# Performance work log

Measured on AMD Instinct MI355X. Metric: run time of the kernel, lower is better.

## Reference

```python
import jax, jax.numpy as jnp
import numpy as np

B, T, C = 2, 2048, 1024
H, D, R = 16, 64, 32  # heads, head_dim, compression rank (R < D)


def setup_inputs() -> dict:
    key = jax.random.key(0)
    ks = jax.random.split(key, 8)
    s = 0.02
    return {
        "hidden_states": jax.random.normal(ks[0], (B, T, C), jnp.float32),
        "c_attn_w": jax.random.normal(ks[1], (C, 3 * C), jnp.float32) * s,
        "c_attn_b": jnp.zeros((3 * C,), jnp.float32),
        "c_proj_w": jax.random.normal(ks[2], (C, C), jnp.float32) * s,
        "c_proj_b": jnp.zeros((C,), jnp.float32),
        "wk_c": jax.random.normal(ks[3], (D, R), jnp.float32) * (1.0 / np.sqrt(D)),
        "wk_e": jax.random.normal(ks[4], (R, D), jnp.float32) * (1.0 / np.sqrt(R)),
        "wv_c": jax.random.normal(ks[5], (D, R), jnp.float32) * (1.0 / np.sqrt(D)),
        "wv_e": jax.random.normal(ks[6], (R, D), jnp.float32) * (1.0 / np.sqrt(R)),
    }


def reference(hidden_states, c_attn_w, c_attn_b, c_proj_w, c_proj_b,
              wk_c, wk_e, wv_c, wv_e):
    b, t, c = hidden_states.shape
    # GPT2 Conv1D: x @ W + b, then split into Q, K, V
    qkv = hidden_states @ c_attn_w + c_attn_b  # [B,T,3C]
    q, k, v = jnp.split(qkv, 3, axis=-1)

    def split_heads(x):  # [B,T,C] -> [B,H,T,D]
        return x.reshape(b, t, H, D).transpose(0, 2, 1, 3)

    q = split_heads(q)
    k = split_heads(k)
    v = split_heads(v)

    # Low-rank KV compression then expansion (rank R < D path)
    k_lat = jnp.einsum('bhtd,dr->bhtr', k, wk_c)  # [B,H,T,R]
    v_lat = jnp.einsum('bhtd,dr->bhtr', v, wv_c)
    k_exp = jnp.einsum('bhtr,rd->bhtd', k_lat, wk_e)  # [B,H,T,D]
    v_exp = jnp.einsum('bhtr,rd->bhtd', v_lat, wv_e)

    # Causal SDPA (attention_mask is None and q_len > 1 -> is_causal=True)
    scale = 1.0 / np.sqrt(D).astype(np.float32)
    scores = jnp.einsum('bhqd,bhkd->bhqk', q, k_exp) * scale  # [B,H,T,T]
    causal = jnp.tril(jnp.ones((t, t), dtype=bool))
    scores = jnp.where(causal[None, None], scores, jnp.finfo(scores.dtype).min)
    probs = jax.nn.softmax(scores, axis=-1)
    attn = jnp.einsum('bhqk,bhkd->bhqd', probs, v_exp)  # [B,H,T,D]

    # Merge heads and output projection
    attn = attn.transpose(0, 2, 1, 3).reshape(b, t, c)
    out = attn @ c_proj_w + c_proj_b
    return out
```

## Files before the change

### kernel.cpp

```cpp
#include <hip/hip_runtime.h>
#include <cstddef>

typedef __attribute__((ext_vector_type(8))) __bf16 bf16x8;
typedef __attribute__((ext_vector_type(4))) float f32x4;
typedef unsigned short u16;
typedef unsigned int   u32;

#define SCLF (0.125f * 1.44269504f)

__device__ __forceinline__ u16 f2bf(float f){
  union { float f; u32 u; } v; v.f = f;
  u32 r = v.u + 0x7FFFu + ((v.u >> 16) & 1u);
  return (u16)(r >> 16);
}
__device__ __forceinline__ u32 cvtpk(float lo, float hi){
  u32 r; asm("v_cvt_pk_bf16_f32 %0, %1, %2" : "=v"(r) : "v"(lo), "v"(hi)); return r;
}
__device__ __forceinline__ void gll16(const void* g, void* l){
  __builtin_amdgcn_global_load_lds((__attribute__((address_space(1))) void*)g,
                                   (__attribute__((address_space(3))) void*)l, 16, 0, 0);
}

__global__ __launch_bounds__(256) void prep_all(const float* __restrict__ x,
      const float* __restrict__ Wa, const float* __restrict__ ba, const float* __restrict__ Wp,
      const float* __restrict__ kc, const float* __restrict__ ke,
      const float* __restrict__ vc, const float* __restrict__ ve,
      u16* __restrict__ Wt, float* __restrict__ b2, u16* __restrict__ W2t,
      u16* __restrict__ Xb){
  __shared__ __align__(16) char PS[40960];
  const int bid = blockIdx.x, tid = threadIdx.x;
  if (bid < 768){
    float* WaL = (float*)PS;
    float* Ws  = (float*)(PS + 16640);
    const int part = bid >> 8, rem = bid & 255, h = rem >> 4, cc = rem & 15;
    #pragma unroll
    for (int i=0;i<8;++i){
      int idx = tid + i*256; int d = idx>>5, r = idx&31;
      Ws[idx] = (part==0) ? ke[r*64+d] : (part==1) ? kc[idx] : vc[idx];
    }
    const int c0 = cc*64, off = part*1024 + h*64;
    {
      int col = tid & 63, rbase = tid >> 6;
      #pragma unroll
      for (int i=0;i<16;++i){
        int row = i*4 + rbase;
        WaL[row*65 + col] = Wa[(size_t)(c0+row)*3072 + off + col];
      }
    }
    __syncthreads();
    const int c = tid & 63, rg = tid >> 6;
    float acc[8] = {};
    for (int d=0; d<64; ++d){
      float a = WaL[c*65 + d];
      #pragma unroll
      for (int rr=0;rr<8;++rr) acc[rr] += a * Ws[d*32 + rg*8 + rr];
    }
    const float scl = (part==0) ? SCLF : 1.f;
    const int nbase = part*512 + h*32 + rg*8;
    #pragma unroll
    for (int rr=0;rr<8;++rr)
      Wt[(size_t)(nbase+rr)*1024 + c0 + c] = f2bf(acc[rr]*scl);
  } else if (bid < 896){
    float* WpL = (float*)PS;
    float* WeL = (float*)(PS + 32768);
    const int idx2 = bid - 768, jc = idx2 & 7, h = idx2 >> 3;
    #pragma unroll
    for (int i=0;i<32;++i){
      int idx = tid + i*256; int d = idx>>7, jj = idx&127;
      WpL[idx] = Wp[(size_t)(h*64+d)*1024 + jc*128 + jj];
    }
    #pragma unroll
    for (int i=0;i<8;++i) WeL[tid + i*256] = ve[tid + i*256];
    __syncthreads();
    const int jj = tid & 127, rg = tid >> 7;
    float out[16] = {};
    #pragma unroll
    for (int d=0; d<64; ++d){
      float pv = WpL[d*128 + jj];
      #pragma unroll
      for (int rr=0; rr<16; ++rr) out[rr] += WeL[(rg*16+rr)*64 + d] * pv;
    }
    #pragma unroll
    for (int rr=0; rr<16; ++rr)
      W2t[(size_t)(jc*128 + jj)*512 + h*32 + rg*16 + rr] = f2bf(out[rr]);
  } else if (bid < 1920){
    const int i0 = (bid - 896)*1024 + tid;
    #pragma unroll
    for (int t=0;t<4;++t){
      int i = i0 + t*256;
      float4 v = ((const float4*)x)[i];
      ushort4 r; r.x = f2bf(v.x); r.y = f2bf(v.y); r.z = f2bf(v.z); r.w = f2bf(v.w);
      ((ushort4*)Xb)[i] = r;
    }
  } else {
    int n = (bid - 1920)*256 + tid;
    int part = n>>9, h = (n>>5)&15, r = n&31;
    const float* bs = ba + part*1024 + h*64;
    float acc = 0.f;
    for (int d=0;d<64;++d){
      float w = (part==0) ? ke[r*64+d] : (part==1) ? kc[d*32+r] : vc[d*32+r];
      acc += bs[d]*w;
    }
    b2[n] = acc * ((part==0) ? SCLF : 1.f);
  }
}

__global__ __launch_bounds__(256) void v_transpose_lat(const u16* __restrict__ QKV,
      u16* __restrict__ Vt){
  __shared__ u16 tile[64][40];
  int tt = blockIdx.x, bh = blockIdx.y;
  int b = bh>>4, h = bh&15;
  int tid = threadIdx.x;
  int row = tid>>2, cc2 = (tid&3)*8;
  const u16* src = QKV + (size_t)(b*2048 + tt*64 + row)*1536 + 1024 + h*32 + cc2;
  *(uint4*)&tile[row][cc2] = *(const uint4*)src;
  __syncthreads();
  int r = tid>>3, pc = (tid&7)*8;
  u16 vals[8];
  #pragma unroll
  for (int i=0;i<8;++i){
    int p = pc+i; int c = p>>5, q = p&31, g = q>>3, j = q&7;
    int o = c*32 + 16*(j>>2) + 4*g + (j&3);
    vals[i] = tile[o][r];
  }
  u16* drow = Vt + (size_t)(bh*32 + r)*2048 + tt*64 + pc;
  *(uint4*)drow = *(const uint4*)&vals[0];
}

template<typename OT>
__global__ __launch_bounds__(256) void gemm64(const u16* __restrict__ A, const u16* __restrict__ Bt,
        const float* __restrict__ bias, OT* __restrict__ C, int M, int N, int K, int ldc){
  __shared__ u16 As[64*64];
  __shared__ u16 Bs[128*64];
  const int nwg = gridDim.x * gridDim.y;
  const int id  = blockIdx.x + gridDim.x * blockIdx.y;
  const int nid = (id & 7) * (nwg >> 3) + (id >> 3);
  const int bx = nid % gridDim.x, by = nid / gridDim.x;
  const int tid = threadIdx.x, wv = tid>>6, ln = tid&63;
  const int lr = ln&15, g8 = (ln>>4)*8;
  const int m0 = bx*64, n0 = by*128;
  const int wr = (wv>>1)*32, wc = (wv&1)*64;
  const int lrow = ln>>3, lcol = (ln&7)*8;
  f32x4 acc[2][4] = {};
  const int nk = K >> 6;
  for (int kt=0; kt<nk; ++kt){
    #pragma unroll
    for (int it=0; it<6; ++it){
      int chunk = wv*6 + it;
      if (chunk < 8){
        int row = chunk*8 + lrow;
        gll16(A + (size_t)(m0+row)*K + kt*64 + lcol, &As[chunk*512]);
      } else {
        int bc = chunk - 8;
        int row = bc*8 + lrow;
        gll16(Bt + (size_t)(n0+row)*K + kt*64 + lcol, &Bs[bc*512]);
      }
    }
    __syncthreads();
    #pragma unroll
    for (int ks=0; ks<2; ++ks){
      bf16x8 af[2], bfr[4];
      #pragma unroll
      for (int mt=0;mt<2;++mt) af[mt]  = *(const bf16x8*)&As[(wr+mt*16+lr)*64 + ks*32 + g8];
      #pragma unroll
      for (int nt=0;nt<4;++nt) bfr[nt] = *(const bf16x8*)&Bs[(wc+nt*16+lr)*64 + ks*32 + g8];
      #pragma unroll
      for (int mt=0;mt<2;++mt)
        #pragma unroll
        for (int nt=0;nt<4;++nt)
          acc[mt][nt] = __builtin_amdgcn_mfma_f32_16x16x32_bf16(af[mt], bfr[nt], acc[mt][nt], 0,0,0);
    }
    __syncthreads();
  }
  #pragma unroll
  for (int mt=0;mt<2;++mt){
    int row = m0 + wr + mt*16 + 4*(ln>>4);
    #pragma unroll
    for (int nt=0;nt<4;++nt){
      int col = n0 + wc + nt*16 + lr;
      float bv = bias[col];
      #pragma unroll
      for (int r=0;r<4;++r){
        float v = acc[mt][nt][r] + bv;
        if constexpr (sizeof(OT) == 2) C[(size_t)(row+r)*ldc + col] = f2bf(v);
        else                           C[(size_t)(row+r)*ldc + col] = v;
      }
    }
  }
}

__global__ __launch_bounds__(512, 8) void attn_fwd(const u16* __restrict__ QKV,
            const u16* __restrict__ Vt, u16* __restrict__ Out){
  const int bh = blockIdx.x;
  const int qt = 31 - blockIdx.y;
  const int b = bh >> 4, h = bh & 15;
  const int tid = threadIdx.x, wv = tid>>6, ln = tid&63;
  const int sg = wv>>2, wvL = wv&3;
  const int lr = ln&15, gq = ln>>4;
  __shared__ __align__(16) char SMEM[32768];
  u16* KB0 = (u16*)SMEM           + (sg*2    )*2048;
  u16* KB1 = (u16*)SMEM           + (sg*2 + 1)*2048;
  u16* VB0 = (u16*)(SMEM + 16384) + (sg*2    )*2048;
  u16* VB1 = (u16*)(SMEM + 16384) + (sg*2 + 1)*2048;
  const int q0 = qt*64;
  const size_t base = (size_t)(b*2048) * 1536;
  bf16x8 qf = *(const bf16x8*)(QKV + base + (size_t)(q0 + wvL*16 + lr)*1536 + h*32 + gq*8);
  const int qglob = q0 + wvL*16 + lr;
  f32x4 o0 = {}, o1 = {};
  float l_r = 0.f;
  const u16* ksrc = QKV + base + 512 + h*32;
  const u16* vsrc = Vt + (size_t)(bh*32)*2048;

  const int ci = wvL*64 + ln;
  const int rK = ci>>2, cK = 8*((ci&3) ^ (rK&3));
  const int rV = ci>>3, cV = 8*((ci&7) ^ (rV&7));

  int offK[4], offV[2][2];
  #pragma unroll
  for (int nt=0;nt<4;++nt)
    offK[nt] = (nt*16+lr)*64 + ((gq*16) ^ ((lr&3)<<4));
  #pragma unroll
  for (int dt=0;dt<2;++dt)
    #pragma unroll
    for (int c=0;c<2;++c)
      offV[dt][c] = (dt*16+lr)*128 + ((c*64 + gq*16) ^ ((lr&7)<<4));

  if (sg <= qt){
    gll16(ksrc + (size_t)(sg*64 + rK)*1536 + cK, KB0 + wvL*512);
    gll16(vsrc + (size_t)rV*2048 + sg*64 + cV,   VB0 + wvL*512);
  }
  __syncthreads();
  const u16* kp = ksrc + (size_t)(sg*64 + 128 + rK)*1536 + cK;
  const u16* vp = vsrc + (size_t)rV*2048 + sg*64 + 128 + cV;
  const size_t KSTEP = (size_t)128*1536;

  #define ABODY(II, KBC, VBC, KBN, VBN) do { \
    const int kt = 2*(II) + sg; \
    if (kt + 2 <= qt){ \
      gll16(kp, (KBN) + wvL*512); \
      gll16(vp, (VBN) + wvL*512); \
      kp += KSTEP; vp += 128; \
    } \
    if (kt <= qt){ \
      f32x4 s4[4] = {}; \
      __builtin_amdgcn_s_setprio(1); \
      _Pragma("unroll") for (int nt=0;nt<4;++nt){ \
        bf16x8 k0 = *(const bf16x8*)((const char*)(KBC) + offK[nt]); \
        s4[nt] = __builtin_amdgcn_mfma_f32_16x16x32_bf16(k0, qf, s4[nt], 0,0,0); \
      } \
      __builtin_amdgcn_s_setprio(0); \
      if (kt == qt){ \
        const int kv0 = kt*64; \
        _Pragma("unroll") for (int nt=0;nt<4;++nt) \
        _Pragma("unroll") for (int r=0;r<4;++r){ \
          int k = kv0 + nt*16 + 4*gq + r; \
          if (k > qglob) s4[nt][r] = -1e30f; \
        } \
      } \
      float p0,p1,p2,p3,p4,p5,p6,p7; \
      p0=__builtin_amdgcn_exp2f(s4[0][0]); p1=__builtin_amdgcn_exp2f(s4[0][1]); \
      p2=__builtin_amdgcn_exp2f(s4[0][2]); p3=__builtin_amdgcn_exp2f(s4[0][3]); \
      p4=__builtin_amdgcn_exp2f(s4[1][0]); p5=__builtin_amdgcn_exp2f(s4[1][1]); \
      p6=__builtin_amdgcn_exp2f(s4[1][2]); p7=__builtin_amdgcn_exp2f(s4[1][3]); \
      l_r += ((p0+p1)+(p2+p3)) + ((p4+p5)+(p6+p7)); \
      union { u32 u[4]; bf16x8 v; } pa0, pa1; \
      pa0.u[0]=cvtpk(p0,p1); pa0.u[1]=cvtpk(p2,p3); pa0.u[2]=cvtpk(p4,p5); pa0.u[3]=cvtpk(p6,p7); \
      p0=__builtin_amdgcn_exp2f(s4[2][0]); p1=__builtin_amdgcn_exp2f(s4[2][1]); \
      p2=__builtin_amdgcn_exp2f(s4[2][2]); p3=__builtin_amdgcn_exp2f(s4[2][3]); \
      p4=__builtin_amdgcn_exp2f(s4[3][0]); p5=__builtin_amdgcn_exp2f(s4[3][1]); \
      p6=__builtin_amdgcn_exp2f(s4[3][2]); p7=__builtin_amdgcn_exp2f(s4[3][3]); \
      l_r += ((p0+p1)+(p2+p3)) + ((p4+p5)+(p6+p7)); \
      pa1.u[0]=cvtpk(p0,p1); pa1.u[1]=cvtpk(p2,p3); pa1.u[2]=cvtpk(p4,p5); pa1.u[3]=cvtpk(p6,p7); \
      __builtin_amdgcn_s_setprio(1); \
      o0 = __builtin_amdgcn_mfma_f32_16x16x32_bf16(pa0.v, *(const bf16x8*)((const char*)(VBC) + offV[0][0]), o0, 0,0,0); \
      o1 = __builtin_amdgcn_mfma_f32_16x16x32_bf16(pa0.v, *(const bf16x8*)((const char*)(VBC) + offV[1][0]), o1, 0,0,0); \
      o0 = __builtin_amdgcn_mfma_f32_16x16x32_bf16(pa1.v, *(const bf16x8*)((const char*)(VBC) + offV[0][1]), o0, 0,0,0); \
      o1 = __builtin_amdgcn_mfma_f32_16x16x32_bf16(pa1.v, *(const bf16x8*)((const char*)(VBC) + offV[1][1]), o1, 0,0,0); \
      __builtin_amdgcn_s_setprio(0); \
    } \
    __syncthreads(); \
  } while(0)

  const int nmax = (qt + 2) >> 1;
  const int jmax = (nmax + 1) >> 1;
  for (int j = 0; j < jmax; ++j){
    ABODY(2*j,   KB0, VB0, KB1, VB1);
    ABODY(2*j+1, KB1, VB1, KB0, VB0);
  }
  l_r += __shfl_xor(l_r, 16);
  l_r += __shfl_xor(l_r, 32);

  float* MO = (float*)SMEM;
  float* ML = (float*)(SMEM + 12288);
  if (sg == 1){
    #pragma unroll
    for (int r=0;r<4;++r){
      MO[(wvL*16 + 4*gq + r)*34 + lr]      = o0[r];
      MO[(wvL*16 + 4*gq + r)*34 + 16 + lr] = o1[r];
    }
    if (gq == 0) ML[wvL*16 + lr] = l_r;
  }
  __syncthreads();
  if (sg == 0){
    float lS = l_r + ML[wvL*16 + lr];
    float lS_o[4];
    #pragma unroll
    for (int r=0;r<4;++r) lS_o[r] = __shfl(lS, 4*gq + r);
    #pragma unroll
    for (int r=0;r<4;++r){
      int orow = wvL*16 + 4*gq + r;
      float v0 = (o0[r] + MO[orow*34 + lr])      / lS_o[r];
      float v1 = (o1[r] + MO[orow*34 + 16 + lr]) / lS_o[r];
      size_t ob = (size_t)(b*2048 + q0 + orow)*512 + h*32;
      Out[ob + lr]      = f2bf(v0);
      Out[ob + 16 + lr] = f2bf(v1);
    }
  }
}

#define WS_B2   0u
#define WS_WT   8192u
#define WS_W2T  (WS_WT + 3145728u)
#define WS_XB   (WS_W2T + 1048576u)
#define WS_QKV  (WS_XB + 8388608u)
#define WS_VT   (WS_QKV + 12582912u)
#define WS_ATT  (WS_VT + 4194304u)

extern "C" void kernel_launch(void* const* d_in, const int* in_sizes, int n_in,
                              void* d_out, int out_size, void* d_ws, size_t ws_size,
                              hipStream_t stream) {
  const float* x  = (const float*)d_in[0];
  const float* Wa = (const float*)d_in[1];
  const float* ba = (const float*)d_in[2];
  const float* Wp = (const float*)d_in[3];
  const float* bp = (const float*)d_in[4];
  const float* kc = (const float*)d_in[5];
  const float* ke = (const float*)d_in[6];
  const float* vc = (const float*)d_in[7];
  const float* ve = (const float*)d_in[8];
  float* out = (float*)d_out;
  char* ws = (char*)d_ws;
  float* b2  = (float*)(ws + WS_B2);
  u16* Wt    = (u16*)(ws + WS_WT);
  u16* W2t   = (u16*)(ws + WS_W2T);
  u16* Xb    = (u16*)(ws + WS_XB);
  u16* QKVb  = (u16*)(ws + WS_QKV);
  u16* Vt    = (u16*)(ws + WS_VT);
  u16* Att   = (u16*)(ws + WS_ATT);

  prep_all<<<1926, 256, 0, stream>>>(x, Wa, ba, Wp, kc, ke, vc, ve, Wt, b2, W2t, Xb);
  gemm64<u16><<<dim3(64,12), 256, 0, stream>>>(Xb, Wt, b2, QKVb, 4096, 1536, 1024, 1536);
  v_transpose_lat<<<dim3(32,32), 256, 0, stream>>>(QKVb, Vt);
  attn_fwd<<<dim3(32,32), 512, 0, stream>>>(QKVb, Vt, Att);
  gemm64<float><<<dim3(64,8), 256, 0, stream>>>(Att, W2t, bp, out, 4096, 1024, 512, 1024);
}
```

Baseline: 86.20 us.

## Fuse fp32-to-bf16 input conversion into QKV GEMM and split prep kernel

Drops the separate conversion of the fp32 hidden states to a bf16 workspace buffer. The QKV GEMM now loads fp32 rows directly, packs them to bf16 in registers and stores them into LDS, while B tiles still use direct global-to-LDS loads. The monolithic prep kernel is split into three kernels for the weight folds and bias fold, with vectorized float4 loads and an LDS-staged bias fold. This saves an 8 MB write and reread of the converted input. In exchange the GEMM reads twice as many A bytes per tile through registers instead of async LDS loads, and there are two extra kernel launches.

```diff
diff --git a/kernel.cpp b/kernel.cpp
--- a/kernel.cpp
+++ b/kernel.cpp
@@ -21,87 +21,112 @@
                                    (__attribute__((address_space(3))) void*)l, 16, 0, 0);
 }
 
-__global__ __launch_bounds__(256) void prep_all(const float* __restrict__ x,
-      const float* __restrict__ Wa, const float* __restrict__ ba, const float* __restrict__ Wp,
+__global__ __launch_bounds__(256) void fold_qkv(const float* __restrict__ Wa,
       const float* __restrict__ kc, const float* __restrict__ ke,
-      const float* __restrict__ vc, const float* __restrict__ ve,
-      u16* __restrict__ Wt, float* __restrict__ b2, u16* __restrict__ W2t,
-      u16* __restrict__ Xb){
-  __shared__ __align__(16) char PS[40960];
-  const int bid = blockIdx.x, tid = threadIdx.x;
-  if (bid < 768){
-    float* WaL = (float*)PS;
-    float* Ws  = (float*)(PS + 16640);
-    const int part = bid >> 8, rem = bid & 255, h = rem >> 4, cc = rem & 15;
-    #pragma unroll
-    for (int i=0;i<8;++i){
-      int idx = tid + i*256; int d = idx>>5, r = idx&31;
-      Ws[idx] = (part==0) ? ke[r*64+d] : (part==1) ? kc[idx] : vc[idx];
-    }
-    const int c0 = cc*64, off = part*1024 + h*64;
-    {
-      int col = tid & 63, rbase = tid >> 6;
-      #pragma unroll
-      for (int i=0;i<16;++i){
-        int row = i*4 + rbase;
-        WaL[row*65 + col] = Wa[(size_t)(c0+row)*3072 + off + col];
-      }
-    }
-    __syncthreads();
-    const int c = tid & 63, rg = tid >> 6;
-    float acc[8] = {};
+      const float* __restrict__ vc, u16* __restrict__ Wt){
+  __shared__ float WaL[64*65];
+  __shared__ float Ws[2048];
+  const int bid = blockIdx.x;
+  const int part = bid >> 8, rem = bid & 255, h = rem >> 4, cc = rem & 15;
+  const int tid = threadIdx.x;
+  {
+    const float* msrc = (part==0) ? ke : (part==1) ? kc : vc;
+    *(float4*)&Ws[tid*4]        = ((const float4*)msrc)[tid];
+    *(float4*)&Ws[1024 + tid*4] = ((const float4*)msrc)[tid + 256];
+  }
+  const int c0 = cc*64, off = part*1024 + h*64;
+  {
+    int r0 = tid >> 4, c4 = (tid & 15) * 4;
+    #pragma unroll
+    for (int i=0;i<4;++i){
+      int row = i*16 + r0;
+      float4 v = *(const float4*)&Wa[(size_t)(c0+row)*3072 + off + c4];
+      WaL[row*65 + c4 + 0] = v.x;
+      WaL[row*65 + c4 + 1] = v.y;
+      WaL[row*65 + c4 + 2] = v.z;
+      WaL[row*65 + c4 + 3] = v.w;
+    }
+  }
+  __syncthreads();
+  const int c = tid & 63, rg = tid >> 6;
+  float acc[8] = {};
+  if (part == 0){
     for (int d=0; d<64; ++d){
       float a = WaL[c*65 + d];
       #pragma unroll
+      for (int rr=0;rr<8;++rr) acc[rr] += a * Ws[(rg*8+rr)*64 + d];
+    }
+  } else {
+    for (int d=0; d<64; ++d){
+      float a = WaL[c*65 + d];
+      #pragma unroll
       for (int rr=0;rr<8;++rr) acc[rr] += a * Ws[d*32 + rg*8 + rr];
     }
-    const float scl = (part==0) ? SCLF : 1.f;
-    const int nbase = part*512 + h*32 + rg*8;
-    #pragma unroll
-    for (int rr=0;rr<8;++rr)
-      Wt[(size_t)(nbase+rr)*1024 + c0 + c] = f2bf(acc[rr]*scl);
-  } else if (bid < 896){
-    float* WpL = (float*)PS;
-    float* WeL = (float*)(PS + 32768);
-    const int idx2 = bid - 768, jc = idx2 & 7, h = idx2 >> 3;
-    #pragma unroll
-    for (int i=0;i<32;++i){
-      int idx = tid + i*256; int d = idx>>7, jj = idx&127;
-      WpL[idx] = Wp[(size_t)(h*64+d)*1024 + jc*128 + jj];
-    }
-    #pragma unroll
-    for (int i=0;i<8;++i) WeL[tid + i*256] = ve[tid + i*256];
-    __syncthreads();
-    const int jj = tid & 127, rg = tid >> 7;
-    float out[16] = {};
-    #pragma unroll
-    for (int d=0; d<64; ++d){
-      float pv = WpL[d*128 + jj];
-      #pragma unroll
-      for (int rr=0; rr<16; ++rr) out[rr] += WeL[(rg*16+rr)*64 + d] * pv;
-    }
-    #pragma unroll
-    for (int rr=0; rr<16; ++rr)
-      W2t[(size_t)(jc*128 + jj)*512 + h*32 + rg*16 + rr] = f2bf(out[rr]);
-  } else if (bid < 1920){
-    const int i0 = (bid - 896)*1024 + tid;
-    #pragma unroll
-    for (int t=0;t<4;++t){
-      int i = i0 + t*256;
-      float4 v = ((const float4*)x)[i];
-      ushort4 r; r.x = f2bf(v.x); r.y = f2bf(v.y); r.z = f2bf(v.z); r.w = f2bf(v.w);
-      ((ushort4*)Xb)[i] = r;
-    }
-  } else {
-    int n = (bid - 1920)*256 + tid;
-    int part = n>>9, h = (n>>5)&15, r = n&31;
-    const float* bs = ba + part*1024 + h*64;
+  }
+  const float scl = (part==0) ? SCLF : 1.f;
+  const int nbase = part*512 + h*32 + rg*8;
+  #pragma unroll
+  for (int rr=0;rr<8;++rr)
+    Wt[(size_t)(nbase+rr)*1024 + c0 + c] = f2bf(acc[rr]*scl);
+}
+
+__global__ __launch_bounds__(256) void fold_proj(const float* __restrict__ Wp,
+      const float* __restrict__ ve, u16* __restrict__ W2t){
+  __shared__ float WpL[8192];
+  __shared__ float WeL[2048];
+  const int jc = blockIdx.x, h = blockIdx.y;
+  const int tid = threadIdx.x;
+  {
+    int dd = tid >> 5, c4 = (tid & 31) * 4;
+    #pragma unroll
+    for (int i=0;i<8;++i){
+      int d = i*8 + dd;
+      *(float4*)&WpL[d*128 + c4] = *(const float4*)&Wp[(size_t)(h*64+d)*1024 + jc*128 + c4];
+    }
+    *(float4*)&WeL[tid*4]        = ((const float4*)ve)[tid];
+    *(float4*)&WeL[1024 + tid*4] = ((const float4*)ve)[tid + 256];
+  }
+  __syncthreads();
+  const int jj = tid & 127, rg = tid >> 7;
+  float out[16] = {};
+  for (int d=0; d<64; ++d){
+    float pv = WpL[d*128 + jj];
+    #pragma unroll
+    for (int rr=0; rr<16; ++rr) out[rr] += WeL[(rg*16+rr)*64 + d] * pv;
+  }
+  #pragma unroll
+  for (int rr=0; rr<16; ++rr)
+    W2t[(size_t)(jc*128 + jj)*512 + h*32 + rg*16 + rr] = f2bf(out[rr]);
+}
+
+__global__ __launch_bounds__(256) void fold_bias(const float* __restrict__ ba,
+      const float* __restrict__ kc, const float* __restrict__ ke,
+      const float* __restrict__ vc, float* __restrict__ b2){
+  __shared__ float BaL[1024];
+  __shared__ float Ws65[32*65];
+  const int part = blockIdx.x, tid = threadIdx.x;
+  *(float4*)&BaL[tid*4] = *(const float4*)&ba[part*1024 + tid*4];
+  {
+    const float* msrc = (part==0) ? ke : (part==1) ? kc : vc;
+    #pragma unroll
+    for (int i=0;i<8;++i){
+      int idx = tid + i*256;
+      float v = msrc[idx];
+      int r, d;
+      if (part == 0){ r = idx >> 6; d = idx & 63; }
+      else          { d = idx >> 5; r = idx & 31; }
+      Ws65[r*65 + d] = v;
+    }
+  }
+  __syncthreads();
+  const float scl = (part==0) ? SCLF : 1.f;
+  #pragma unroll
+  for (int t=0;t<2;++t){
+    int l = tid + t*256;
+    int hh = l >> 5, r = l & 31;
     float acc = 0.f;
-    for (int d=0;d<64;++d){
-      float w = (part==0) ? ke[r*64+d] : (part==1) ? kc[d*32+r] : vc[d*32+r];
-      acc += bs[d]*w;
-    }
-    b2[n] = acc * ((part==0) ? SCLF : 1.f);
+    for (int d=0;d<64;++d) acc += BaL[hh*64 + d] * Ws65[r*65 + d];
+    b2[part*512 + l] = acc * scl;
   }
 }
 
@@ -127,8 +152,8 @@
   *(uint4*)drow = *(const uint4*)&vals[0];
 }
 
-template<typename OT>
-__global__ __launch_bounds__(256) void gemm64(const u16* __restrict__ A, const u16* __restrict__ Bt,
+template<typename AT, typename OT>
+__global__ __launch_bounds__(256) void gemm64(const AT* __restrict__ A, const u16* __restrict__ Bt,
         const float* __restrict__ bias, OT* __restrict__ C, int M, int N, int K, int ldc){
   __shared__ u16 As[64*64];
   __shared__ u16 Bs[128*64];
@@ -144,16 +169,36 @@
   f32x4 acc[2][4] = {};
   const int nk = K >> 6;
   for (int kt=0; kt<nk; ++kt){
-    #pragma unroll
-    for (int it=0; it<6; ++it){
-      int chunk = wv*6 + it;
-      if (chunk < 8){
-        int row = chunk*8 + lrow;
-        gll16(A + (size_t)(m0+row)*K + kt*64 + lcol, &As[chunk*512]);
-      } else {
-        int bc = chunk - 8;
-        int row = bc*8 + lrow;
-        gll16(Bt + (size_t)(n0+row)*K + kt*64 + lcol, &Bs[bc*512]);
+    if constexpr (sizeof(AT) == 4){
+      int row = tid>>2, seg = (tid&3)*16;
+      const float* xs = (const float*)A + (size_t)(m0+row)*K + kt*64 + seg;
+      float4 a0 = ((const float4*)xs)[0], a1 = ((const float4*)xs)[1],
+             a2 = ((const float4*)xs)[2], a3 = ((const float4*)xs)[3];
+      uint4 w0, w1;
+      w0.x = cvtpk(a0.x,a0.y); w0.y = cvtpk(a0.z,a0.w);
+      w0.z = cvtpk(a1.x,a1.y); w0.w = cvtpk(a1.z,a1.w);
+      w1.x = cvtpk(a2.x,a2.y); w1.y = cvtpk(a2.z,a2.w);
+      w1.z = cvtpk(a3.x,a3.y); w1.w = cvtpk(a3.z,a3.w);
+      *(uint4*)&As[row*64 + seg]     = w0;
+      *(uint4*)&As[row*64 + seg + 8] = w1;
+      #pragma unroll
+      for (int it=0; it<4; ++it){
+        int bc = wv*4 + it;
+        int rowb = bc*8 + lrow;
+        gll16(Bt + (size_t)(n0+rowb)*K + kt*64 + lcol, &Bs[bc*512]);
+      }
+    } else {
+      #pragma unroll
+      for (int it=0; it<6; ++it){
+        int chunk = wv*6 + it;
+        if (chunk < 8){
+          int row = chunk*8 + lrow;
+          gll16((const u16*)A + (size_t)(m0+row)*K + kt*64 + lcol, &As[chunk*512]);
+        } else {
+          int bc = chunk - 8;
+          int row = bc*8 + lrow;
+          gll16(Bt + (size_t)(n0+row)*K + kt*64 + lcol, &Bs[bc*512]);
+        }
       }
     }
     __syncthreads();
@@ -321,8 +366,7 @@
 #define WS_B2   0u
 #define WS_WT   8192u
 #define WS_W2T  (WS_WT + 3145728u)
-#define WS_XB   (WS_W2T + 1048576u)
-#define WS_QKV  (WS_XB + 8388608u)
+#define WS_QKV  (WS_W2T + 1048576u)
 #define WS_VT   (WS_QKV + 12582912u)
 #define WS_ATT  (WS_VT + 4194304u)
 
@@ -343,14 +387,15 @@
   float* b2  = (float*)(ws + WS_B2);
   u16* Wt    = (u16*)(ws + WS_WT);
   u16* W2t   = (u16*)(ws + WS_W2T);
-  u16* Xb    = (u16*)(ws + WS_XB);
   u16* QKVb  = (u16*)(ws + WS_QKV);
   u16* Vt    = (u16*)(ws + WS_VT);
   u16* Att   = (u16*)(ws + WS_ATT);
 
-  prep_all<<<1926, 256, 0, stream>>>(x, Wa, ba, Wp, kc, ke, vc, ve, Wt, b2, W2t, Xb);
-  gemm64<u16><<<dim3(64,12), 256, 0, stream>>>(Xb, Wt, b2, QKVb, 4096, 1536, 1024, 1536);
+  fold_bias<<<3, 256, 0, stream>>>(ba, kc, ke, vc, b2);
+  fold_proj<<<dim3(8,16), 256, 0, stream>>>(Wp, ve, W2t);
+  fold_qkv<<<768, 256, 0, stream>>>(Wa, kc, ke, vc, Wt);
+  gemm64<float,u16><<<dim3(64,12), 256, 0, stream>>>(x, Wt, b2, QKVb, 4096, 1536, 1024, 1536);
   v_transpose_lat<<<dim3(32,32), 256, 0, stream>>>(QKVb, Vt);
   attn_fwd<<<dim3(32,32), 512, 0, stream>>>(QKVb, Vt, Att);
-  gemm64<float><<<dim3(64,8), 256, 0, stream>>>(Att, W2t, bp, out, 4096, 1024, 512, 1024);
-}
+  gemm64<u16,float><<<dim3(64,8), 256, 0, stream>>>(Att, W2t, bp, out, 4096, 1024, 512, 1024);
+}
```

After: 91.62 us. 6.3% more time.
